# Kernel optimization log

Hardware: AMD Instinct MI355X
Metric: run time of the kernel (lower is better)

## Reference

```python
import jax, jax.numpy as jnp
import numpy as np
import math

B, S, D, H, N, DFF = 16, 512, 512, 8, 6, 2048
NBUCK, MAXD = 32, 10.0


def _ln(x, g, b, eps=1e-5):
    mu = jnp.mean(x, axis=-1, keepdims=True)
    var = jnp.mean(jnp.square(x - mu), axis=-1, keepdims=True)
    return (x - mu) * jax.lax.rsqrt(var + eps) * g + b


def setup_inputs() -> dict:
    key = jax.random.key(0)
    ks = jax.random.split(key, 10)
    inp = {
        "x": jax.random.normal(ks[0], (B, S, D), jnp.float32),
        "coordinates": jax.random.uniform(ks[1], (S - 1, 2), jnp.float32) * 16.0,
        "cls_pe": jax.random.normal(ks[2], (1, D), jnp.float32) * 0.02,
        "bias_emb": jax.random.normal(ks[3], (NBUCK, H), jnp.float32) * 0.02,
        "attn_w": jax.random.normal(ks[4], (N, 4, D, D), jnp.float32) * 0.02,
        "attn_b": jnp.zeros((N, 4, D), jnp.float32),
        "ff_w1": jax.random.normal(ks[5], (N, D, DFF), jnp.float32) * 0.02,
        "ff_b1": jnp.zeros((N, DFF), jnp.float32),
        "ff_w2": jax.random.normal(ks[6], (N, DFF, D), jnp.float32) * 0.02,
        "ff_b2": jnp.zeros((N, D), jnp.float32),
        "ln_g": jnp.ones((N, 2, D), jnp.float32),
        "ln_b": jnp.zeros((N, 2, D), jnp.float32),
        "norm_g": jnp.ones((D,), jnp.float32),
        "norm_b": jnp.zeros((D,), jnp.float32),
        "norm2_g": jnp.ones((D,), jnp.float32),
        "norm2_b": jnp.zeros((D,), jnp.float32),
        "mask": jnp.zeros((B, 1, 1, S), jnp.bool_),
    }
    return inp


def _pe2d(coordinates, cls_pe, d_model):
    # PositionalEncoding2D: separate sin/cos for x and y coords
    half = d_model // 2
    div = jnp.exp(jnp.arange(0, half, 2, dtype=jnp.float32) * (-math.log(10000.0) / half))
    n = coordinates.shape[0]
    xa = coordinates[:, :1] * div  # [n, half//2]
    ya = coordinates[:, 1:2] * div
    pe_x = jnp.zeros((n, half), coordinates.dtype).at[:, 0::2].set(jnp.sin(xa)).at[:, 1::2].set(jnp.cos(xa))
    pe_y = jnp.zeros((n, half), coordinates.dtype).at[:, 0::2].set(jnp.sin(ya)).at[:, 1::2].set(jnp.cos(ya))
    pe = jnp.concatenate([pe_x, pe_y], axis=-1)  # [n, D]
    return jnp.concatenate([cls_pe, pe], axis=0)  # [1+n, D] with CLS slot


def _rel_pos_bias(coordinates, bias_emb, n_heads, seq_len):
    # RelativePositionBias: bucketized pairwise 2D distance -> per-head bias
    diff = coordinates[:, None, :] - coordinates[None, :, :]
    dist = jnp.linalg.norm(diff, axis=-1)
    buckets = (jnp.clip(dist / MAXD, 0.0, 1.0) * (NBUCK - 1)).astype(jnp.int32)
    bias = bias_emb[buckets]                       # [n, n, H]
    bias = jnp.transpose(bias, (2, 0, 1))          # [H, n, n]
    pad = seq_len - bias.shape[-1]
    bias = jnp.pad(bias, ((0, 0), (pad, 0), (pad, 0)))  # zero bias for CLS
    return bias[None]                              # [1, H, S, S]


def reference(x, coordinates, cls_pe, bias_emb, attn_w, attn_b, ff_w1, ff_b1,
              ff_w2, ff_b2, ln_g, ln_b, norm_g, norm_b, norm2_g, norm2_b, mask):
    b, s, d = x.shape
    h = bias_emb.shape[1]
    dk = d // h
    scale = 1.0 / math.sqrt(dk)

    x = x + _pe2d(coordinates, cls_pe, d)[None]
    bias = _rel_pos_bias(coordinates, bias_emb, h, s)

    def mha(xin, W, bb):
        q = (xin @ W[0] + bb[0]).reshape(b, s, h, dk).swapaxes(1, 2)
        k = (xin @ W[1] + bb[1]).reshape(b, s, h, dk).swapaxes(1, 2)
        v = (xin @ W[2] + bb[2]).reshape(b, s, h, dk).swapaxes(1, 2)
        scores = jnp.einsum('bhqd,bhkd->bhqk', q, k) * scale + bias
        scores = jnp.where(mask, -1e9, scores)
        p = jax.nn.softmax(scores, axis=-1)
        o = jnp.einsum('bhqk,bhkd->bhqd', p, v).swapaxes(1, 2).reshape(b, s, d)
        return o @ W[3] + bb[3]

    n_layers = attn_w.shape[0]
    for i in range(n_layers):
        x = x + mha(_ln(x, ln_g[i, 0], ln_b[i, 0]), attn_w[i], attn_b[i])
        hdn = _ln(x, ln_g[i, 1], ln_b[i, 1])
        x = x + (jax.nn.gelu(hdn @ ff_w1[i] + ff_b1[i], approximate=False) @ ff_w2[i] + ff_b2[i])
        if (i + 1) == n_layers // 2 and n_layers > 1:
            x = _ln(x, norm2_g, norm2_b)
    return _ln(x, norm_g, norm_b)
```

## Files before the change

### kernel.cpp

```cpp
#include <hip/hip_runtime.h>
#include <cstdint>
#include <cstddef>

#define B_ 16
#define S_ 512
#define D_ 512
#define H_ 8
#define DK_ 64
#define NL_ 6
#define DFF_ 2048

typedef float f32x4 __attribute__((ext_vector_type(4)));
typedef __bf16 bf16x8 __attribute__((ext_vector_type(8)));
typedef unsigned short u16x8 __attribute__((ext_vector_type(8)));

__device__ __forceinline__ unsigned short f2bf(float f) {
  unsigned u = __builtin_bit_cast(unsigned, f);
  unsigned r = (u + 0x7FFFu + ((u >> 16) & 1u)) >> 16;
  return (unsigned short)r;
}
__device__ __forceinline__ float bf2f(unsigned short v) {
  unsigned u = ((unsigned)v) << 16;
  return __builtin_bit_cast(float, u);
}

__device__ __forceinline__ void gl_lds16(const unsigned short* g, unsigned short* l) {
  __builtin_amdgcn_global_load_lds(
      (const __attribute__((address_space(1))) unsigned int*)g,
      (__attribute__((address_space(3))) unsigned int*)l, 16, 0, 0);
}

__global__ __launch_bounds__(256) void pe_add_kernel(const float* __restrict__ x,
                                                     const float* __restrict__ coords,
                                                     const float* __restrict__ cls_pe,
                                                     float* __restrict__ xo) {
  int idx = blockIdx.x * 256 + threadIdx.x;
  int d = idx & (D_ - 1);
  int s = (idx >> 9) & (S_ - 1);
  float pe;
  if (s == 0) {
    pe = cls_pe[d];
  } else {
    float c = coords[(s - 1) * 2 + (d >= 256 ? 1 : 0)];
    int dd = d & 255;
    int t = dd >> 1;
    float ang = c * expf((float)t * -0.07195578415606394f);
    pe = (dd & 1) ? cosf(ang) : sinf(ang);
  }
  xo[idx] = x[idx] + pe;
}

__global__ __launch_bounds__(256) void bias_kernel(const float* __restrict__ coords,
                                                   const float* __restrict__ emb,
                                                   unsigned short* __restrict__ bias) {
  int idx = blockIdx.x * 256 + threadIdx.x;
  int j = idx & (S_ - 1), i = idx >> 9;
  unsigned short v[H_];
  if (i == 0 || j == 0) {
#pragma unroll
    for (int h = 0; h < H_; h++) v[h] = 0;
  } else {
    float dx = coords[(i - 1) * 2] - coords[(j - 1) * 2];
    float dy = coords[(i - 1) * 2 + 1] - coords[(j - 1) * 2 + 1];
    float dist = sqrtf(dx * dx + dy * dy);
    float t = fminf(dist / 10.0f, 1.0f) * 31.0f;
    int bkt = (int)t;
#pragma unroll
    for (int h = 0; h < H_; h++) v[h] = f2bf(emb[bkt * H_ + h]);
  }
#pragma unroll
  for (int h = 0; h < H_; h++) bias[(size_t)h * S_ * S_ + idx] = v[h];
}

__global__ __launch_bounds__(256) void transpose_cvt(const float* __restrict__ src,
                                                     unsigned short* __restrict__ dst,
                                                     int R, int C) {
  src += (size_t)blockIdx.z * R * C;
  dst += (size_t)blockIdx.z * R * C;
  __shared__ float tile[32][33];
  int tx = threadIdx.x & 31, ty = threadIdx.x >> 5;
  int c0 = blockIdx.x * 32, r0 = blockIdx.y * 32;
#pragma unroll
  for (int i = 0; i < 32; i += 8)
    tile[ty + i][tx] = src[(size_t)(r0 + ty + i) * C + c0 + tx];
  __syncthreads();
#pragma unroll
  for (int i = 0; i < 32; i += 8)
    dst[(size_t)(c0 + ty + i) * R + r0 + tx] = f2bf(tile[tx][ty + i]);
}

template <int OUTMODE>
__global__ __launch_bounds__(256) void ln_kernel(const float* __restrict__ x,
                                                 const float* __restrict__ g,
                                                 const float* __restrict__ be,
                                                 void* __restrict__ out) {
  int wid = threadIdx.x >> 6, l = threadIdx.x & 63;
  size_t row = (size_t)blockIdx.x * 4 + wid;
  const float4* xr = reinterpret_cast<const float4*>(x + row * D_);
  float4 a = xr[l * 2], c = xr[l * 2 + 1];
  float s = a.x + a.y + a.z + a.w + c.x + c.y + c.z + c.w;
  float sq = a.x * a.x + a.y * a.y + a.z * a.z + a.w * a.w +
             c.x * c.x + c.y * c.y + c.z * c.z + c.w * c.w;
#pragma unroll
  for (int m = 1; m < 64; m <<= 1) {
    s += __shfl_xor(s, m);
    sq += __shfl_xor(sq, m);
  }
  float mean = s * (1.0f / D_);
  float var = sq * (1.0f / D_) - mean * mean;
  float rstd = rsqrtf(var + 1e-5f);
  const float4* gp = reinterpret_cast<const float4*>(g);
  const float4* bp = reinterpret_cast<const float4*>(be);
  float4 g0 = gp[l * 2], g1 = gp[l * 2 + 1];
  float4 b0 = bp[l * 2], b1 = bp[l * 2 + 1];
  float y[8];
  y[0] = (a.x - mean) * rstd * g0.x + b0.x;
  y[1] = (a.y - mean) * rstd * g0.y + b0.y;
  y[2] = (a.z - mean) * rstd * g0.z + b0.z;
  y[3] = (a.w - mean) * rstd * g0.w + b0.w;
  y[4] = (c.x - mean) * rstd * g1.x + b1.x;
  y[5] = (c.y - mean) * rstd * g1.y + b1.y;
  y[6] = (c.z - mean) * rstd * g1.z + b1.z;
  y[7] = (c.w - mean) * rstd * g1.w + b1.w;
  if (OUTMODE == 0) {
    u16x8 o;
#pragma unroll
    for (int j = 0; j < 8; j++) o[j] = f2bf(y[j]);
    *reinterpret_cast<u16x8*>((unsigned short*)out + row * D_ + l * 8) = o;
  } else {
    float4 o0 = {y[0], y[1], y[2], y[3]};
    float4 o1 = {y[4], y[5], y[6], y[7]};
    float4* op = reinterpret_cast<float4*>((float*)out + row * D_ + l * 8);
    op[0] = o0;
    op[1] = o1;
  }
}

template <int EPI, int BK>
__global__ __launch_bounds__(256) void gemm_bt(const unsigned short* __restrict__ A,
                                               const unsigned short* __restrict__ BT,
                                               const float* __restrict__ bias,
                                               unsigned short* __restrict__ outb,
                                               float* __restrict__ resid,
                                               int M, int N, int K) {
  constexpr int TPR = BK / 8;
  constexpr int RPR = 256 / TPR;
  constexpr int ROUNDS = 128 / RPR;
  __shared__ __align__(16) unsigned short As[2][128 * BK];
  __shared__ __align__(16) unsigned short Bs[2][128 * BK];
  int tid = threadIdx.x;
  int l = tid & 63, wid = tid >> 6;
  int wr = wid >> 1, wc = wid & 1;

  int nwg = gridDim.x * gridDim.y;
  int flat = blockIdx.y * gridDim.x + blockIdx.x;
  int cpx = nwg >> 3;
  int work = (flat & 7) * cpx + (flat >> 3);
  int bx = work % gridDim.x, by = work / gridDim.x;
  int m0 = by * 128, n0 = bx * 128;
  int lr = l & 15, lk = (l >> 4) * 8;

  f32x4 acc[4][4];
#pragma unroll
  for (int m = 0; m < 4; m++)
#pragma unroll
    for (int n = 0; n < 4; n++) acc[m][n] = f32x4{0.f, 0.f, 0.f, 0.f};

  int sr = tid / TPR;
  int sc8 = (tid % TPR) * 8;
  const unsigned short* Ag = A + (size_t)(m0 + sr) * K + sc8;
  const unsigned short* Bg = BT + (size_t)(n0 + sr) * K + sc8;

  auto stage = [&](int c, int k0) {
#pragma unroll
    for (int i = 0; i < ROUNDS; i++) {
      gl_lds16(Ag + (size_t)(i * RPR) * K + k0, &As[c][(sr + i * RPR) * BK + sc8]);
      gl_lds16(Bg + (size_t)(i * RPR) * K + k0, &Bs[c][(sr + i * RPR) * BK + sc8]);
    }
  };
  auto compute = [&](int c) {
#pragma unroll
    for (int ks = 0; ks < BK / 32; ks++) {
      bf16x8 af[4], bfr[4];
#pragma unroll
      for (int m = 0; m < 4; m++)
        af[m] = *reinterpret_cast<const bf16x8*>(&As[c][(wr * 64 + m * 16 + lr) * BK + ks * 32 + lk]);
#pragma unroll
      for (int n = 0; n < 4; n++)
        bfr[n] = *reinterpret_cast<const bf16x8*>(&Bs[c][(wc * 64 + n * 16 + lr) * BK + ks * 32 + lk]);
#pragma unroll
      for (int m = 0; m < 4; m++)
#pragma unroll
        for (int n = 0; n < 4; n++)
          acc[m][n] = __builtin_amdgcn_mfma_f32_16x16x32_bf16(af[m], bfr[n], acc[m][n], 0, 0, 0);
    }
  };

  const int nt = K / BK;
  stage(0, 0);
  __syncthreads();
  int cur = 0;
  for (int t = 0; t < nt; ++t) {
    if (t + 1 < nt) stage(cur ^ 1, (t + 1) * BK);
    compute(cur);
    __syncthreads();
    cur ^= 1;
  }

#pragma unroll
  for (int m = 0; m < 4; m++) {
#pragma unroll
    for (int n = 0; n < 4; n++) {
      int gc = n0 + wc * 64 + n * 16 + lr;
      float bv = bias[gc];
#pragma unroll
      for (int rr = 0; rr < 4; rr++) {
        int gr = m0 + wr * 64 + m * 16 + (l >> 4) * 4 + rr;
        float v = acc[m][n][rr] + bv;
        if (EPI == 0) {
          outb[(size_t)gr * N + gc] = f2bf(v);
        } else if (EPI == 1) {
          resid[(size_t)gr * N + gc] += v;
        } else if (EPI == 2) {
          float gl = 0.5f * v * (1.0f + erff(v * 0.70710678118654752f));
          outb[(size_t)gr * N + gc] = f2bf(gl);
        } else {
          if (gc < 512) {
            outb[(size_t)gr * 512 + gc] = f2bf(v);
          } else if (gc < 1024) {
            (outb + 4194304)[(size_t)gr * 512 + (gc - 512)] = f2bf(v);
          } else {
            int c = gc - 1024;
            int h = c >> 6, dd = c & 63, bb = gr >> 9, ss = gr & 511;
            (outb + 8388608)[((size_t)((bb * H_ + h) * DK_ + dd)) * S_ + ss] = f2bf(v);
          }
        }
      }
    }
  }
}

__global__ __launch_bounds__(256) void attn_kernel(const unsigned short* __restrict__ Q,
                                                   const unsigned short* __restrict__ K,
                                                   const unsigned short* __restrict__ VT,
                                                   const unsigned short* __restrict__ bias,
                                                   const unsigned char* __restrict__ mask,
                                                   unsigned short* __restrict__ O) {
  __shared__ __align__(16) unsigned short Ks[128 * 64];
  __shared__ __align__(16) unsigned short Vs[64 * 128];
  __shared__ __align__(16) unsigned short P[4][16 * 136];
  int tid = threadIdx.x;
  int wid = tid >> 6, l = tid & 63;
  int bh = blockIdx.x;
  int b = bh >> 3, h = bh & 7;
  int q0 = blockIdx.y * 64 + wid * 16;
  int lr = l & 15;
  int lk = (l >> 4) * 8;
  int rb = (l >> 4) * 4;

  const unsigned short* qp = Q + (size_t)(b * S_ + q0 + lr) * D_ + h * DK_ + lk;
  bf16x8 aq0 = *reinterpret_cast<const bf16x8*>(qp);
  bf16x8 aq1 = *reinterpret_cast<const bf16x8*>(qp + 32);

  f32x4 ao[4];
#pragma unroll
  for (int n = 0; n < 4; n++) ao[n] = f32x4{0.f, 0.f, 0.f, 0.f};
  float m_[4] = {-3.0e38f, -3.0e38f, -3.0e38f, -3.0e38f};
  float l_[4] = {0.f, 0.f, 0.f, 0.f};

  for (int t = 0; t < 4; t++) {
    int s0 = t * 128;
    __syncthreads();
#pragma unroll
    for (int i = 0; i < 4; i++) {
      int c = (wid * 4 + i) * 64 + l;
      int krow = c >> 3, kjs = c & 7, kj = kjs ^ (krow & 7);
      gl_lds16(K + (size_t)(b * S_ + s0 + krow) * D_ + h * DK_ + kj * 8, &Ks[c * 8]);
      int dk = c >> 4, vjs = c & 15, vj = vjs ^ (dk & 7);
      gl_lds16(VT + (size_t)(bh * DK_ + dk) * S_ + s0 + vj * 8, &Vs[c * 8]);
    }
    __syncthreads();

    f32x4 sc[8];
#pragma unroll
    for (int n = 0; n < 8; n++) sc[n] = f32x4{0.f, 0.f, 0.f, 0.f};
#pragma unroll
    for (int n = 0; n < 8; n++) {
      int r = n * 16 + lr;
      bf16x8 k0 = *reinterpret_cast<const bf16x8*>(&Ks[r * 64 + (((l >> 4)) ^ (r & 7)) * 8]);
      bf16x8 k1 = *reinterpret_cast<const bf16x8*>(&Ks[r * 64 + ((4 + (l >> 4)) ^ (r & 7)) * 8]);
      sc[n] = __builtin_amdgcn_mfma_f32_16x16x32_bf16(aq0, k0, sc[n], 0, 0, 0);
      sc[n] = __builtin_amdgcn_mfma_f32_16x16x32_bf16(aq1, k1, sc[n], 0, 0, 0);
    }

    const unsigned short* bp = bias + ((size_t)h * S_ + q0 + rb) * S_ + s0;
    float pmax[4] = {-3.0e38f, -3.0e38f, -3.0e38f, -3.0e38f};
#pragma unroll
    for (int n = 0; n < 8; n++) {
      int scn = n * 16 + lr;
      bool msk = mask[b * S_ + s0 + scn] != 0;
#pragma unroll
      for (int rr = 0; rr < 4; rr++) {
        float v = sc[n][rr] * 0.125f + bf2f(bp[(size_t)rr * S_ + scn]);
        v = msk ? -1e9f : v;
        sc[n][rr] = v;
        pmax[rr] = fmaxf(pmax[rr], v);
      }
    }
#pragma unroll
    for (int rr = 0; rr < 4; rr++) {
#pragma unroll
      for (int mm = 1; mm < 16; mm <<= 1) pmax[rr] = fmaxf(pmax[rr], __shfl_xor(pmax[rr], mm));
    }
    float scl[4], psum[4];
#pragma unroll
    for (int rr = 0; rr < 4; rr++) {
      float mn = fmaxf(m_[rr], pmax[rr]);
      scl[rr] = __expf(m_[rr] - mn);
      m_[rr] = mn;
      psum[rr] = 0.f;
    }
#pragma unroll
    for (int n = 0; n < 8; n++) {
#pragma unroll
      for (int rr = 0; rr < 4; rr++) {
        float p = __expf(sc[n][rr] - m_[rr]);
        psum[rr] += p;
        P[wid][(rb + rr) * 136 + n * 16 + lr] = f2bf(p);
      }
    }
#pragma unroll
    for (int rr = 0; rr < 4; rr++) {
#pragma unroll
      for (int mm = 1; mm < 16; mm <<= 1) psum[rr] += __shfl_xor(psum[rr], mm);
      l_[rr] = l_[rr] * scl[rr] + psum[rr];
    }
#pragma unroll
    for (int n = 0; n < 4; n++)
#pragma unroll
      for (int rr = 0; rr < 4; rr++) ao[n][rr] *= scl[rr];

#pragma unroll
    for (int kk = 0; kk < 4; kk++) {
      bf16x8 pa = *reinterpret_cast<const bf16x8*>(&P[wid][lr * 136 + kk * 32 + lk]);
#pragma unroll
      for (int n = 0; n < 4; n++) {
        int dk = n * 16 + lr;
        bf16x8 vb = *reinterpret_cast<const bf16x8*>(&Vs[dk * 128 + ((kk * 4 + (l >> 4)) ^ (dk & 7)) * 8]);
        ao[n] = __builtin_amdgcn_mfma_f32_16x16x32_bf16(pa, vb, ao[n], 0, 0, 0);
      }
    }
  }

  float inv[4];
#pragma unroll
  for (int rr = 0; rr < 4; rr++) inv[rr] = 1.0f / l_[rr];
#pragma unroll
  for (int n = 0; n < 4; n++)
#pragma unroll
    for (int rr = 0; rr < 4; rr++)
      O[(size_t)(b * S_ + q0 + rb + rr) * D_ + h * DK_ + n * 16 + lr] = f2bf(ao[n][rr] * inv[rr]);
}

extern "C" void kernel_launch(void* const* d_in, const int* in_sizes, int n_in,
                              void* d_out, int out_size, void* d_ws, size_t ws_size,
                              hipStream_t stream) {
  const float* x = (const float*)d_in[0];
  const float* coords = (const float*)d_in[1];
  const float* cls_pe = (const float*)d_in[2];
  const float* bias_emb = (const float*)d_in[3];
  const float* attn_w = (const float*)d_in[4];
  const float* attn_b = (const float*)d_in[5];
  const float* ff_w1 = (const float*)d_in[6];
  const float* ff_b1 = (const float*)d_in[7];
  const float* ff_w2 = (const float*)d_in[8];
  const float* ff_b2 = (const float*)d_in[9];
  const float* ln_g = (const float*)d_in[10];
  const float* ln_b = (const float*)d_in[11];
  const float* norm_g = (const float*)d_in[12];
  const float* norm_b = (const float*)d_in[13];
  const float* norm2_g = (const float*)d_in[14];
  const float* norm2_b = (const float*)d_in[15];
  const unsigned char* mask = (const unsigned char*)d_in[16];

  char* ws = (char*)d_ws;
  float* xf = (float*)(ws + 0);
  unsigned short* biasbuf = (unsigned short*)(ws + 16777216);
  unsigned short* wattnT = (unsigned short*)(ws + 25165824);
  unsigned short* wff1T = (unsigned short*)(ws + 37748736);
  unsigned short* wff2T = (unsigned short*)(ws + 50331648);
  unsigned short* lnbuf = (unsigned short*)(ws + 62914560);
  unsigned short* Qb = (unsigned short*)(ws + 71303168);
  unsigned short* Kb = (unsigned short*)(ws + 79691776);
  unsigned short* VTb = (unsigned short*)(ws + 88080384);
  unsigned short* Ob = (unsigned short*)(ws + 96468992);
  unsigned short* H1b = Qb;

  const int M = B_ * S_;

  pe_add_kernel<<<(B_ * S_ * D_) / 256, 256, 0, stream>>>(x, coords, cls_pe, xf);
  bias_kernel<<<(S_ * S_) / 256, 256, 0, stream>>>(coords, bias_emb, biasbuf);
  transpose_cvt<<<dim3(16, 16, 24), 256, 0, stream>>>(attn_w, wattnT, 512, 512);
  transpose_cvt<<<dim3(64, 16, 6), 256, 0, stream>>>(ff_w1, wff1T, 512, 2048);
  transpose_cvt<<<dim3(16, 64, 6), 256, 0, stream>>>(ff_w2, wff2T, 2048, 512);

  for (int i = 0; i < NL_; i++) {
    ln_kernel<0><<<M / 4, 256, 0, stream>>>(xf, ln_g + (i * 2 + 0) * D_, ln_b + (i * 2 + 0) * D_, lnbuf);
    gemm_bt<4, 32><<<dim3(12, 64), 256, 0, stream>>>(lnbuf, wattnT + (size_t)(i * 4 + 0) * D_ * D_,
                                                     attn_b + (i * 4 + 0) * D_, Qb, nullptr, M, 1536, D_);
    attn_kernel<<<dim3(B_ * H_, 8), 256, 0, stream>>>(Qb, Kb, VTb, biasbuf, mask, Ob);
    gemm_bt<1, 64><<<dim3(4, 64), 256, 0, stream>>>(Ob, wattnT + (size_t)(i * 4 + 3) * D_ * D_,
                                                    attn_b + (i * 4 + 3) * D_, nullptr, xf, M, D_, D_);
    ln_kernel<0><<<M / 4, 256, 0, stream>>>(xf, ln_g + (i * 2 + 1) * D_, ln_b + (i * 2 + 1) * D_, lnbuf);
    gemm_bt<2, 32><<<dim3(16, 64), 256, 0, stream>>>(lnbuf, wff1T + (size_t)i * DFF_ * D_,
                                                     ff_b1 + i * DFF_, H1b, nullptr, M, DFF_, D_);
    gemm_bt<1, 64><<<dim3(4, 64), 256, 0, stream>>>(H1b, wff2T + (size_t)i * D_ * DFF_,
                                                    ff_b2 + i * D_, nullptr, xf, M, D_, DFF_);
    if (i == 2) ln_kernel<1><<<M / 4, 256, 0, stream>>>(xf, norm2_g, norm2_b, xf);
  }
  ln_kernel<1><<<M / 4, 256, 0, stream>>>(xf, norm_g, norm_b, (float*)d_out);
}
```

Measured before the change: 1.443 ms.

## Add 256x256 GEMM tiles, split-K FF2 with atomics, and MFMA-ordered bias layout

Adds a 512-thread GEMM kernel with 256x256 tiles, used for the QKV and FF1 projections to raise data reuse per block. The FF2 GEMM now uses split-K over 4 slices and accumulates into the residual with float atomics, which gives more blocks for its long K dimension. The relative-position bias is stored in the per-lane MFMA order, so the attention kernel loads it with one vector load per row instead of scattered scalar loads. In exchange, the atomic accumulation makes summation order nondeterministic and adds atomic traffic, and the large tiles use more registers and LDS.

```diff
diff --git a/kernel.cpp b/kernel.cpp
--- a/kernel.cpp
+++ b/kernel.cpp
@@ -68,8 +68,10 @@
 #pragma unroll
     for (int h = 0; h < H_; h++) v[h] = f2bf(emb[bkt * H_ + h]);
   }
-#pragma unroll
-  for (int h = 0; h < H_; h++) bias[(size_t)h * S_ * S_ + idx] = v[h];
+  int t = j >> 7, w = j & 127, plr = w & 15, pn = w >> 4;
+#pragma unroll
+  for (int h = 0; h < H_; h++)
+    bias[(((size_t)h * S_ + i) * 4 + t) * 128 + plr * 8 + pn] = v[h];
 }
 
 __global__ __launch_bounds__(256) void transpose_cvt(const float* __restrict__ src,
@@ -136,7 +138,32 @@
   }
 }
 
-template <int EPI, int BK>
+template <int EPI, int SPLIT>
+__device__ __forceinline__ void gemm_epi(float v, int gr, int gc, int N, int split,
+                                         const float* bias, unsigned short* outb,
+                                         float* resid) {
+  if (EPI == 0) {
+    outb[(size_t)gr * N + gc] = f2bf(v);
+  } else if (EPI == 1) {
+    if (SPLIT == 1) resid[(size_t)gr * N + gc] += v;
+    else atomicAdd(&resid[(size_t)gr * N + gc], v);
+  } else if (EPI == 2) {
+    float gl = 0.5f * v * (1.0f + erff(v * 0.70710678118654752f));
+    outb[(size_t)gr * N + gc] = f2bf(gl);
+  } else {
+    if (gc < 512) {
+      outb[(size_t)gr * 512 + gc] = f2bf(v);
+    } else if (gc < 1024) {
+      (outb + 4194304)[(size_t)gr * 512 + (gc - 512)] = f2bf(v);
+    } else {
+      int c = gc - 1024;
+      int h = c >> 6, dd = c & 63, bb = gr >> 9, ss = gr & 511;
+      (outb + 8388608)[((size_t)((bb * H_ + h) * DK_ + dd)) * S_ + ss] = f2bf(v);
+    }
+  }
+}
+
+template <int EPI, int BK, int SPLIT>
 __global__ __launch_bounds__(256) void gemm_bt(const unsigned short* __restrict__ A,
                                                const unsigned short* __restrict__ BT,
                                                const float* __restrict__ bias,
@@ -159,6 +186,7 @@
   int bx = work % gridDim.x, by = work / gridDim.x;
   int m0 = by * 128, n0 = bx * 128;
   int lr = l & 15, lk = (l >> 4) * 8;
+  int kbase = blockIdx.z * (K / SPLIT);
 
   f32x4 acc[4][4];
 #pragma unroll
@@ -168,8 +196,8 @@
 
   int sr = tid / TPR;
   int sc8 = (tid % TPR) * 8;
-  const unsigned short* Ag = A + (size_t)(m0 + sr) * K + sc8;
-  const unsigned short* Bg = BT + (size_t)(n0 + sr) * K + sc8;
+  const unsigned short* Ag = A + (size_t)(m0 + sr) * K + kbase + sc8;
+  const unsigned short* Bg = BT + (size_t)(n0 + sr) * K + kbase + sc8;
 
   auto stage = [&](int c, int k0) {
 #pragma unroll
@@ -196,7 +224,7 @@
     }
   };
 
-  const int nt = K / BK;
+  const int nt = K / SPLIT / BK;
   stage(0, 0);
   __syncthreads();
   int cur = 0;
@@ -212,29 +240,94 @@
 #pragma unroll
     for (int n = 0; n < 4; n++) {
       int gc = n0 + wc * 64 + n * 16 + lr;
-      float bv = bias[gc];
+      float bv = (SPLIT == 1 || blockIdx.z == 0) ? bias[gc] : 0.f;
 #pragma unroll
       for (int rr = 0; rr < 4; rr++) {
         int gr = m0 + wr * 64 + m * 16 + (l >> 4) * 4 + rr;
-        float v = acc[m][n][rr] + bv;
-        if (EPI == 0) {
-          outb[(size_t)gr * N + gc] = f2bf(v);
-        } else if (EPI == 1) {
-          resid[(size_t)gr * N + gc] += v;
-        } else if (EPI == 2) {
-          float gl = 0.5f * v * (1.0f + erff(v * 0.70710678118654752f));
-          outb[(size_t)gr * N + gc] = f2bf(gl);
-        } else {
-          if (gc < 512) {
-            outb[(size_t)gr * 512 + gc] = f2bf(v);
-          } else if (gc < 1024) {
-            (outb + 4194304)[(size_t)gr * 512 + (gc - 512)] = f2bf(v);
-          } else {
-            int c = gc - 1024;
-            int h = c >> 6, dd = c & 63, bb = gr >> 9, ss = gr & 511;
-            (outb + 8388608)[((size_t)((bb * H_ + h) * DK_ + dd)) * S_ + ss] = f2bf(v);
-          }
-        }
+        gemm_epi<EPI, SPLIT>(acc[m][n][rr] + bv, gr, gc, N, blockIdx.z, bias, outb, resid);
+      }
+    }
+  }
+}
+
+template <int EPI>
+__global__ __launch_bounds__(512, 2) void gemm256(const unsigned short* __restrict__ A,
+                                                  const unsigned short* __restrict__ BT,
+                                                  const float* __restrict__ bias,
+                                                  unsigned short* __restrict__ outb,
+                                                  float* __restrict__ resid,
+                                                  int M, int N, int K) {
+  __shared__ __align__(16) unsigned short As[2][256 * 64];
+  __shared__ __align__(16) unsigned short Bs[2][256 * 64];
+  int tid = threadIdx.x;
+  int l = tid & 63, wid = tid >> 6;
+  int wr = wid >> 2, wc = wid & 3;
+
+  int nwg = gridDim.x * gridDim.y;
+  int flat = blockIdx.y * gridDim.x + blockIdx.x;
+  int cpx = nwg >> 3;
+  int work = (flat & 7) * cpx + (flat >> 3);
+  int bx = work % gridDim.x, by = work / gridDim.x;
+  int m0 = by * 256, n0 = bx * 256;
+  int lr = l & 15, lk = (l >> 4) * 8;
+
+  f32x4 acc[8][4];
+#pragma unroll
+  for (int m = 0; m < 8; m++)
+#pragma unroll
+    for (int n = 0; n < 4; n++) acc[m][n] = f32x4{0.f, 0.f, 0.f, 0.f};
+
+  int sr = tid >> 3;
+  int sc8 = (tid & 7) * 8;
+  const unsigned short* Ag = A + (size_t)(m0 + sr) * K + sc8;
+  const unsigned short* Bg = BT + (size_t)(n0 + sr) * K + sc8;
+
+  auto stage = [&](int c, int k0) {
+#pragma unroll
+    for (int i = 0; i < 4; i++) {
+      gl_lds16(Ag + (size_t)(i * 64) * K + k0, &As[c][(sr + i * 64) * 64 + sc8]);
+      gl_lds16(Bg + (size_t)(i * 64) * K + k0, &Bs[c][(sr + i * 64) * 64 + sc8]);
+    }
+  };
+  auto compute = [&](int c) {
+#pragma unroll
+    for (int ks = 0; ks < 2; ks++) {
+      bf16x8 af[8], bfr[4];
+#pragma unroll
+      for (int m = 0; m < 8; m++)
+        af[m] = *reinterpret_cast<const bf16x8*>(&As[c][(wr * 128 + m * 16 + lr) * 64 + ks * 32 + lk]);
+#pragma unroll
+      for (int n = 0; n < 4; n++)
+        bfr[n] = *reinterpret_cast<const bf16x8*>(&Bs[c][(wc * 64 + n * 16 + lr) * 64 + ks * 32 + lk]);
+#pragma unroll
+      for (int m = 0; m < 8; m++)
+#pragma unroll
+        for (int n = 0; n < 4; n++)
+          acc[m][n] = __builtin_amdgcn_mfma_f32_16x16x32_bf16(af[m], bfr[n], acc[m][n], 0, 0, 0);
+    }
+  };
+
+  const int nt = K >> 6;
+  stage(0, 0);
+  __syncthreads();
+  int cur = 0;
+  for (int t = 0; t < nt; ++t) {
+    if (t + 1 < nt) stage(cur ^ 1, (t + 1) * 64);
+    compute(cur);
+    __syncthreads();
+    cur ^= 1;
+  }
+
+#pragma unroll
+  for (int m = 0; m < 8; m++) {
+#pragma unroll
+    for (int n = 0; n < 4; n++) {
+      int gc = n0 + wc * 64 + n * 16 + lr;
+      float bv = bias[gc];
+#pragma unroll
+      for (int rr = 0; rr < 4; rr++) {
+        int gr = m0 + wr * 128 + m * 16 + (l >> 4) * 4 + rr;
+        gemm_epi<EPI, 1>(acc[m][n][rr] + bv, gr, gc, N, 0, bias, outb, resid);
       }
     }
   }
@@ -293,7 +386,12 @@
       sc[n] = __builtin_amdgcn_mfma_f32_16x16x32_bf16(aq1, k1, sc[n], 0, 0, 0);
     }
 
-    const unsigned short* bp = bias + ((size_t)h * S_ + q0 + rb) * S_ + s0;
+    u16x8 bvv[4];
+#pragma unroll
+    for (int rr = 0; rr < 4; rr++)
+      bvv[rr] = *reinterpret_cast<const u16x8*>(
+          bias + (((size_t)h * S_ + (q0 + rb + rr)) * 4 + t) * 128 + lr * 8);
+
     float pmax[4] = {-3.0e38f, -3.0e38f, -3.0e38f, -3.0e38f};
 #pragma unroll
     for (int n = 0; n < 8; n++) {
@@ -301,7 +399,7 @@
       bool msk = mask[b * S_ + s0 + scn] != 0;
 #pragma unroll
       for (int rr = 0; rr < 4; rr++) {
-        float v = sc[n][rr] * 0.125f + bf2f(bp[(size_t)rr * S_ + scn]);
+        float v = sc[n][rr] * 0.125f + bf2f(bvv[rr][n]);
         v = msk ? -1e9f : v;
         sc[n][rr] = v;
         pmax[rr] = fmaxf(pmax[rr], v);
@@ -406,16 +504,16 @@
 
   for (int i = 0; i < NL_; i++) {
     ln_kernel<0><<<M / 4, 256, 0, stream>>>(xf, ln_g + (i * 2 + 0) * D_, ln_b + (i * 2 + 0) * D_, lnbuf);
-    gemm_bt<4, 32><<<dim3(12, 64), 256, 0, stream>>>(lnbuf, wattnT + (size_t)(i * 4 + 0) * D_ * D_,
-                                                     attn_b + (i * 4 + 0) * D_, Qb, nullptr, M, 1536, D_);
+    gemm256<4><<<dim3(6, 32), 512, 0, stream>>>(lnbuf, wattnT + (size_t)(i * 4 + 0) * D_ * D_,
+                                                attn_b + (i * 4 + 0) * D_, Qb, nullptr, M, 1536, D_);
     attn_kernel<<<dim3(B_ * H_, 8), 256, 0, stream>>>(Qb, Kb, VTb, biasbuf, mask, Ob);
-    gemm_bt<1, 64><<<dim3(4, 64), 256, 0, stream>>>(Ob, wattnT + (size_t)(i * 4 + 3) * D_ * D_,
-                                                    attn_b + (i * 4 + 3) * D_, nullptr, xf, M, D_, D_);
+    gemm_bt<1, 64, 1><<<dim3(4, 64), 256, 0, stream>>>(Ob, wattnT + (size_t)(i * 4 + 3) * D_ * D_,
+                                                       attn_b + (i * 4 + 3) * D_, nullptr, xf, M, D_, D_);
     ln_kernel<0><<<M / 4, 256, 0, stream>>>(xf, ln_g + (i * 2 + 1) * D_, ln_b + (i * 2 + 1) * D_, lnbuf);
-    gemm_bt<2, 32><<<dim3(16, 64), 256, 0, stream>>>(lnbuf, wff1T + (size_t)i * DFF_ * D_,
-                                                     ff_b1 + i * DFF_, H1b, nullptr, M, DFF_, D_);
-    gemm_bt<1, 64><<<dim3(4, 64), 256, 0, stream>>>(H1b, wff2T + (size_t)i * D_ * DFF_,
-                                                    ff_b2 + i * D_, nullptr, xf, M, D_, DFF_);
+    gemm256<2><<<dim3(8, 32), 512, 0, stream>>>(lnbuf, wff1T + (size_t)i * DFF_ * D_,
+                                                ff_b1 + i * DFF_, H1b, nullptr, M, DFF_, D_);
+    gemm_bt<1, 32, 4><<<dim3(4, 64, 4), 256, 0, stream>>>(H1b, wff2T + (size_t)i * D_ * DFF_,
+                                                          ff_b2 + i * D_, nullptr, xf, M, D_, DFF_);
     if (i == 2) ln_kernel<1><<<M / 4, 256, 0, stream>>>(xf, norm2_g, norm2_b, xf);
   }
   ln_kernel<1><<<M / 4, 256, 0, stream>>>(xf, norm_g, norm_b, (float*)d_out);
```

New measurement: 1.581 ms. 9.5% more time.
